# Optimization experiments

Measured on AMD Instinct MI355X. Metric: run time of the kernel, lower is better.

Reference implementation:

```python
import jax, jax.numpy as jnp
import numpy as np

N_NODES = 100000
N_EDGES = 3200000
NUM_FEATURES = 128
DIM = 10
NUM_GRAPHS = 64


def setup_inputs() -> dict:
    key = jax.random.key(0)
    k1, k2, k3, k4, k5, k6, k7 = jax.random.split(key, 7)
    features = jax.random.normal(k1, (N_NODES, NUM_FEATURES), dtype=jnp.float32)
    src = jax.random.randint(k2, (N_EDGES,), 0, N_NODES, dtype=jnp.int64)
    dst = jax.random.randint(k3, (N_EDGES,), 0, N_NODES, dtype=jnp.int64)
    graph_ids = jnp.sort(jax.random.randint(k4, (N_NODES,), 0, NUM_GRAPHS, dtype=jnp.int64))
    # GraphConv weights (no bias), glorot-ish scaling
    W1 = jax.random.normal(k5, (NUM_FEATURES, DIM), dtype=jnp.float32) / np.sqrt(NUM_FEATURES)
    W2 = jax.random.normal(k6, (DIM, DIM), dtype=jnp.float32) / np.sqrt(DIM)
    W3 = jax.random.normal(k7, (DIM, 1), dtype=jnp.float32) / np.sqrt(DIM)
    return {"features": features, "W1": W1, "W2": W2, "W3": W3,
            "src": src, "dst": dst, "graph_ids": graph_ids}


def _sum_aggregate(h, src, dst, n_nodes):
    # message = h[src], reduce-sum at dst (norm='none' GraphConv aggregation)
    return jax.ops.segment_sum(h[src], dst, num_segments=n_nodes)


def reference(features, W1, W2, W3, src, dst, graph_ids):
    n = features.shape[0]
    # conv1: in_feats(128) > out_feats(10) -> weight first, then aggregate
    h = features @ W1                          # [N, DIM]
    h = _sum_aggregate(h, src, dst, n)         # [N, DIM]
    h = jax.nn.relu(h)
    # conv2: in_feats == out_feats -> aggregate first, then weight
    h = _sum_aggregate(h, src, dst, n) @ W2    # [N, DIM]
    # dgl.mean_nodes: per-graph mean pooling over nodes
    sums = jax.ops.segment_sum(h, graph_ids, num_segments=NUM_GRAPHS)           # [G, DIM]
    cnt = jax.ops.segment_sum(jnp.ones((n, 1), h.dtype), graph_ids, num_segments=NUM_GRAPHS)
    pooled = sums / jnp.maximum(cnt, 1.0)      # [G, DIM]
    return jax.nn.sigmoid(pooled @ W3)         # [G, 1]
```

## Files before the change

kernel.cpp:

```cpp
#include <hip/hip_runtime.h>
#include <hip/hip_fp16.h>

#define N_NODES 100000
#define N_EDGES 3200000
#define NUM_FEATURES 128
#define DIM 10
#define NUM_GRAPHS 64

#define BSHIFT 8
#define BSIZE (1 << BSHIFT)
#define NB ((N_NODES + BSIZE - 1) / BSIZE)
#define CHUNKS 4
#define PCHUNKS 4
#define EPB 6250
#define PLACE_BLOCKS 512
#define NQUAD 25000
#define GEMM_BLOCKS 1563
#define BOUND_BLOCKS 196
#define TILE (BSIZE * DIM)
#define CAP 2560
#define CAPB 16384
#define NCHUNK (NB * CHUNKS)
#define NCHUNK2 (NB * PCHUNKS)
#define ACC_STRIDE 11

#define DPP_ROR_ADD(v, n)                                                        \
    (v) += __int_as_float(__builtin_amdgcn_update_dpp(                           \
        0, __float_as_int(v), 0x120 | (n), 0xF, 0xF, false))

__global__ __launch_bounds__(512) void k_front(const float* __restrict__ feat,
                                               const float* __restrict__ W1,
                                               __half* __restrict__ h1,
                                               const int* __restrict__ gids,
                                               int* __restrict__ bound,
                                               const int* __restrict__ src,
                                               const int* __restrict__ dst,
                                               int* __restrict__ cnt,
                                               int* __restrict__ pk) {
    __shared__ int hd[NB];
    __shared__ int cb[NB];

    if (blockIdx.x < PLACE_BLOCKS) {
        int base0 = blockIdx.x * EPB;
        for (int t = threadIdx.x; t < NB; t += 512) hd[t] = 0;
        __syncthreads();

        {
            int i = threadIdx.x;
            for (; i + 1536 < EPB; i += 2048) {
                int d0 = dst[base0 + i],        d1 = dst[base0 + i + 512];
                int d2 = dst[base0 + i + 1024], d3 = dst[base0 + i + 1536];
                atomicAdd(&hd[d0 >> BSHIFT], 1);
                atomicAdd(&hd[d1 >> BSHIFT], 1);
                atomicAdd(&hd[d2 >> BSHIFT], 1);
                atomicAdd(&hd[d3 >> BSHIFT], 1);
            }
            for (; i < EPB; i += 512)
                atomicAdd(&hd[dst[base0 + i] >> BSHIFT], 1);
        }
        __syncthreads();

        for (int t = threadIdx.x; t < NB; t += 512) {
            int c = hd[t];
            int o = c ? atomicAdd(&cnt[t], c) : 0;
            cb[t] = t * CAPB + o;
        }
        __syncthreads();

        {
            int i = threadIdx.x;
            for (; i + 1536 < EPB; i += 2048) {
                int d0 = dst[base0 + i],        d1 = dst[base0 + i + 512];
                int d2 = dst[base0 + i + 1024], d3 = dst[base0 + i + 1536];
                int s0 = src[base0 + i],        s1 = src[base0 + i + 512];
                int s2 = src[base0 + i + 1024], s3 = src[base0 + i + 1536];
                int q0 = atomicAdd(&cb[d0 >> BSHIFT], 1);
                int q1 = atomicAdd(&cb[d1 >> BSHIFT], 1);
                int q2 = atomicAdd(&cb[d2 >> BSHIFT], 1);
                int q3 = atomicAdd(&cb[d3 >> BSHIFT], 1);
                if (q0 < ((d0 >> BSHIFT) + 1) * CAPB) pk[q0] = ((d0 & (BSIZE - 1)) << 17) | s0;
                if (q1 < ((d1 >> BSHIFT) + 1) * CAPB) pk[q1] = ((d1 & (BSIZE - 1)) << 17) | s1;
                if (q2 < ((d2 >> BSHIFT) + 1) * CAPB) pk[q2] = ((d2 & (BSIZE - 1)) << 17) | s2;
                if (q3 < ((d3 >> BSHIFT) + 1) * CAPB) pk[q3] = ((d3 & (BSIZE - 1)) << 17) | s3;
            }
            for (; i < EPB; i += 512) {
                int d = dst[base0 + i];
                int s = src[base0 + i];
                int q = atomicAdd(&cb[d >> BSHIFT], 1);
                if (q < ((d >> BSHIFT) + 1) * CAPB) pk[q] = ((d & (BSIZE - 1)) << 17) | s;
            }
        }
        return;
    }

    int bb = blockIdx.x - PLACE_BLOCKS;

    int nb2 = bb * 512 + threadIdx.x;
    if (bb < BOUND_BLOCKS && nb2 < N_NODES) {
        int g  = gids[nb2];
        int gp = nb2 ? gids[nb2 - 1] : -1;
        for (int v = gp + 1; v <= g; ++v) bound[v] = nb2;
        if (nb2 == N_NODES - 1)
            for (int v = g + 1; v <= NUM_GRAPHS; ++v) bound[v] = N_NODES;
    }

    int gid  = bb * 512 + threadIdx.x;
    int quad = gid >> 5;
    int lane = gid & 31;
    if (quad >= NQUAD) return;

    float wf[40];
    {
        const float4* W14 = reinterpret_cast<const float4*>(W1 + lane * 40);
#pragma unroll
        for (int m = 0; m < 10; ++m) {
            float4 q = W14[m];
            wf[4 * m]     = q.x;
            wf[4 * m + 1] = q.y;
            wf[4 * m + 2] = q.z;
            wf[4 * m + 3] = q.w;
        }
    }

    int nbase = quad * 4;
    float4 f[4];
#pragma unroll
    for (int n = 0; n < 4; ++n)
        f[n] = *reinterpret_cast<const float4*>(feat + (size_t)(nbase + n) * NUM_FEATURES + lane * 4);

    float acc[4][DIM];
#pragma unroll
    for (int n = 0; n < 4; ++n)
#pragma unroll
        for (int k = 0; k < DIM; ++k) acc[n][k] = 0.f;

#pragma unroll
    for (int n = 0; n < 4; ++n) {
        float fv[4] = {f[n].x, f[n].y, f[n].z, f[n].w};
#pragma unroll
        for (int j = 0; j < 4; ++j)
#pragma unroll
            for (int k = 0; k < DIM; ++k)
                acc[n][k] += fv[j] * wf[j * DIM + k];
    }

#pragma unroll
    for (int n = 0; n < 4; ++n)
#pragma unroll
        for (int k = 0; k < DIM; ++k) {
            float v = acc[n][k];
            DPP_ROR_ADD(v, 1);
            DPP_ROR_ADD(v, 2);
            DPP_ROR_ADD(v, 4);
            DPP_ROR_ADD(v, 8);
            acc[n][k] = v + __shfl_xor(v, 16);
        }

    if (lane == 0) {
        __half2* o = (__half2*)h1;
#pragma unroll
        for (int n = 0; n < 4; ++n)
#pragma unroll
            for (int j = 0; j < 5; ++j)
                o[(size_t)(nbase + n) * 5 + j] = __floats2half2_rn(acc[n][2 * j], acc[n][2 * j + 1]);
    }
}

__global__ __launch_bounds__(512) void k_spmm1(const __half* __restrict__ h,
                                               const int* __restrict__ cnt,
                                               const int* __restrict__ pk,
                                               float* __restrict__ part) {
    __shared__ int eh[CAP];
    __shared__ int srt[CAP];
    __shared__ int hist[BSIZE];
    __shared__ int cur[BSIZE];

    int b     = blockIdx.x / CHUNKS;
    int chunk = blockIdx.x % CHUNKS;
    int s0  = b * CAPB;
    int len = cnt[b];
    int c0  = s0 + (len * chunk) / CHUNKS;
    int c1  = s0 + (len * (chunk + 1)) / CHUNKS;
    int n   = c1 - c0;
    int nc  = min(n, CAP);

    for (int t = threadIdx.x; t < BSIZE; t += 512) hist[t] = 0;
    __syncthreads();

    {
        int i = threadIdx.x;
        for (; i + 1536 < nc; i += 2048) {
            int p0 = pk[c0 + i],        p1 = pk[c0 + i + 512];
            int p2 = pk[c0 + i + 1024], p3 = pk[c0 + i + 1536];
            eh[i] = p0; eh[i + 512] = p1; eh[i + 1024] = p2; eh[i + 1536] = p3;
            atomicAdd(&hist[p0 >> 17], 1);
            atomicAdd(&hist[p1 >> 17], 1);
            atomicAdd(&hist[p2 >> 17], 1);
            atomicAdd(&hist[p3 >> 17], 1);
        }
        for (; i < nc; i += 512) {
            int p = pk[c0 + i];
            eh[i] = p;
            atomicAdd(&hist[p >> 17], 1);
        }
    }
    __syncthreads();

    if (threadIdx.x < 64) {
        int l = threadIdx.x;
        int carry = 0;
#pragma unroll
        for (int j = 0; j < 4; ++j) {
            int x = hist[j * 64 + l];
            int v = x;
#pragma unroll
            for (int off = 1; off < 64; off <<= 1) {
                int t2 = __shfl_up(v, off);
                if (l >= off) v += t2;
            }
            cur[j * 64 + l] = carry + v - x;
            carry += __shfl(v, 63);
        }
    }
    __syncthreads();

    for (int i = threadIdx.x; i < nc; i += 512) {
        int p = eh[i];
        int pos = atomicAdd(&cur[p >> 17], 1);
        srt[pos] = p;
    }
    __syncthreads();

    int wave = threadIdx.x >> 6;
    int lane = threadIdx.x & 63;
    int slot = lane / 5;
    int l    = lane - slot * 5;
    float* pb = part + (size_t)blockIdx.x * TILE;
    const __half2* h2 = (const __half2*)h;

    if (slot < 12) {
        int g = wave * 12 + slot;
        for (int loc = g; loc < BSIZE; loc += 96) {
            int e0 = loc ? cur[loc - 1] : 0;
            int e1 = cur[loc];
            float ax0 = 0.f, ay0 = 0.f, ax1 = 0.f, ay1 = 0.f;
            float ax2 = 0.f, ay2 = 0.f, ax3 = 0.f, ay3 = 0.f;
            int e = e0;
            for (; e + 7 < e1; e += 8) {
                float2 v0 = __half22float2(h2[(size_t)(srt[e]     & 0x1FFFF) * 5 + l]);
                float2 v1 = __half22float2(h2[(size_t)(srt[e + 1] & 0x1FFFF) * 5 + l]);
                float2 v2 = __half22float2(h2[(size_t)(srt[e + 2] & 0x1FFFF) * 5 + l]);
                float2 v3 = __half22float2(h2[(size_t)(srt[e + 3] & 0x1FFFF) * 5 + l]);
                float2 v4 = __half22float2(h2[(size_t)(srt[e + 4] & 0x1FFFF) * 5 + l]);
                float2 v5 = __half22float2(h2[(size_t)(srt[e + 5] & 0x1FFFF) * 5 + l]);
                float2 v6 = __half22float2(h2[(size_t)(srt[e + 6] & 0x1FFFF) * 5 + l]);
                float2 v7 = __half22float2(h2[(size_t)(srt[e + 7] & 0x1FFFF) * 5 + l]);
                ax0 += v0.x + v4.x; ay0 += v0.y + v4.y;
                ax1 += v1.x + v5.x; ay1 += v1.y + v5.y;
                ax2 += v2.x + v6.x; ay2 += v2.y + v6.y;
                ax3 += v3.x + v7.x; ay3 += v3.y + v7.y;
            }
            for (; e < e1; ++e) {
                float2 v = __half22float2(h2[(size_t)(srt[e] & 0x1FFFF) * 5 + l]);
                ax0 += v.x; ay0 += v.y;
            }
            pb[loc * DIM + 2 * l]     = (ax0 + ax1) + (ax2 + ax3);
            pb[loc * DIM + 2 * l + 1] = (ay0 + ay1) + (ay2 + ay3);
        }
    }
    __syncthreads();

    for (int i = CAP + threadIdx.x; i < n; i += 512) {
        int p = pk[c0 + i];
        int loc = p >> 17, s = p & 0x1FFFF;
#pragma unroll
        for (int j = 0; j < 5; ++j) {
            float2 v = __half22float2(h2[(size_t)s * 5 + j]);
            atomicAdd(&pb[loc * DIM + 2 * j], v.x);
            atomicAdd(&pb[loc * DIM + 2 * j + 1], v.y);
        }
    }
}

__global__ __launch_bounds__(256) void k_merge_relu(const float* __restrict__ part,
                                                    __half* __restrict__ r) {
    int b     = blockIdx.x;
    int nbase = b << BSHIFT;
    const float* p0 = part + (size_t)(b * CHUNKS) * TILE;
    __half2* r2 = (__half2*)r;
    for (int t = threadIdx.x; t < TILE / 2; t += 256) {
        float sx = 0.f, sy = 0.f;
#pragma unroll
        for (int c = 0; c < CHUNKS; ++c) {
            float2 v = ((const float2*)(p0 + (size_t)c * TILE))[t];
            sx += v.x; sy += v.y;
        }
        int ebase = nbase * DIM + 2 * t;
        if (ebase < N_NODES * DIM)
            r2[(size_t)nbase * 5 + t] = __floats2half2_rn(fmaxf(sx, 0.f), fmaxf(sy, 0.f));
    }
}

__global__ __launch_bounds__(512) void k_pass2(const __half* __restrict__ r,
                                               const int* __restrict__ cnt,
                                               const int* __restrict__ pk,
                                               const int* __restrict__ bound,
                                               float* __restrict__ sums) {
    __shared__ float acc[NUM_GRAPHS * ACC_STRIDE];

    int b     = blockIdx.x / PCHUNKS;
    int chunk = blockIdx.x % PCHUNKS;
    int nbase = b << BSHIFT;
    int nlast = min(nbase + BSIZE - 1, N_NODES - 1);

    int glo = 0, ghx = NUM_GRAPHS - 1;
#pragma unroll
    for (int it = 0; it < 6; ++it) {
        int mid = (glo + ghx + 1) >> 1;
        if (bound[mid] <= nbase) glo = mid; else ghx = mid - 1;
    }
    int lo2 = 0, hi2 = NUM_GRAPHS - 1;
#pragma unroll
    for (int it = 0; it < 6; ++it) {
        int mid = (lo2 + hi2 + 1) >> 1;
        if (bound[mid] <= nlast) lo2 = mid; else hi2 = mid - 1;
    }
    int ghi  = lo2;
    int span = ghi - glo;

    for (int t = threadIdx.x; t < (span + 1) * DIM; t += 512)
        acc[(glo + t / DIM) * ACC_STRIDE + t % DIM] = 0.f;
    __syncthreads();

    int s0  = b * CAPB;
    int len = cnt[b];
    int c0  = s0 + (len * chunk) / PCHUNKS;
    int c1  = s0 + (len * (chunk + 1)) / PCHUNKS;

    int wave = threadIdx.x >> 6;
    int lane = threadIdx.x & 63;
    int slot = lane / 5;
    int l    = lane - slot * 5;
    const __half2* r2 = (const __half2*)r;

    if (slot < 12) {
        const int STR = 96;
        int q = wave * 12 + slot;
        int e = c0 + q;
        if (span <= 1) {
            int gA  = glo;
            int gB  = (span == 1) ? glo + 1 : glo;
            int cut = (span == 1) ? (bound[glo + 1] - nbase) : BSIZE;
            float axA = 0.f, ayA = 0.f, axB = 0.f, ayB = 0.f;
            for (; e + 7 * STR < c1; e += 8 * STR) {
                int p[8];
#pragma unroll
                for (int u = 0; u < 8; ++u) p[u] = pk[e + u * STR];
                float2 v[8];
#pragma unroll
                for (int u = 0; u < 8; ++u)
                    v[u] = __half22float2(r2[(size_t)(p[u] & 0x1FFFF) * 5 + l]);
#pragma unroll
                for (int u = 0; u < 8; ++u) {
                    bool a = (p[u] >> 17) < cut;
                    axA += a ? v[u].x : 0.f;  ayA += a ? v[u].y : 0.f;
                    axB += a ? 0.f : v[u].x;  ayB += a ? 0.f : v[u].y;
                }
            }
            for (; e < c1; e += STR) {
                int p = pk[e];
                float2 v = __half22float2(r2[(size_t)(p & 0x1FFFF) * 5 + l]);
                bool a = (p >> 17) < cut;
                axA += a ? v.x : 0.f;  ayA += a ? v.y : 0.f;
                axB += a ? 0.f : v.x;  ayB += a ? 0.f : v.y;
            }
            atomicAdd(&acc[gA * ACC_STRIDE + 2 * l], axA);
            atomicAdd(&acc[gA * ACC_STRIDE + 2 * l + 1], ayA);
            if (span == 1) {
                atomicAdd(&acc[gB * ACC_STRIDE + 2 * l], axB);
                atomicAdd(&acc[gB * ACC_STRIDE + 2 * l + 1], ayB);
            }
        } else {
            for (; e < c1; e += STR) {
                int p   = pk[e];
                int loc = p >> 17;
                float2 v = __half22float2(r2[(size_t)(p & 0x1FFFF) * 5 + l]);
                int g = glo;
                for (int gg = glo + 1; gg <= ghi; ++gg)
                    g += (loc >= bound[gg] - nbase) ? 1 : 0;
                atomicAdd(&acc[g * ACC_STRIDE + 2 * l], v.x);
                atomicAdd(&acc[g * ACC_STRIDE + 2 * l + 1], v.y);
            }
        }
    }
    __syncthreads();

    for (int t = threadIdx.x; t < (span + 1) * DIM; t += 512) {
        int g = glo + t / DIM;
        float v = acc[g * ACC_STRIDE + t % DIM];
        if (v != 0.f) atomicAdd(&sums[g * DIM + t % DIM], v);
    }
}

__global__ void k_final(const float* __restrict__ sums, const int* __restrict__ bound,
                        const float* __restrict__ W2, const float* __restrict__ W3,
                        float* __restrict__ out) {
    int g = threadIdx.x;
    if (g >= NUM_GRAPHS) return;
    float c = fmaxf((float)(bound[g + 1] - bound[g]), 1.f);
    float p[DIM];
#pragma unroll
    for (int k = 0; k < DIM; ++k) p[k] = sums[g * DIM + k] / c;
    float z = 0.f;
#pragma unroll
    for (int j = 0; j < DIM; ++j) {
        float t = 0.f;
#pragma unroll
        for (int k = 0; k < DIM; ++k) t += p[k] * W2[k * DIM + j];
        z += t * W3[j];
    }
    out[g] = 1.f / (1.f + expf(-z));
}

extern "C" void kernel_launch(void* const* d_in, const int* in_sizes, int n_in,
                              void* d_out, int out_size, void* d_ws, size_t ws_size,
                              hipStream_t stream) {
    const float* feat = (const float*)d_in[0];
    const float* W1   = (const float*)d_in[1];
    const float* W2   = (const float*)d_in[2];
    const float* W3   = (const float*)d_in[3];
    const int*   src  = (const int*)d_in[4];
    const int*   dst  = (const int*)d_in[5];
    const int*   gids = (const int*)d_in[6];
    float*       out  = (float*)d_out;

    char* ws = (char*)d_ws;
    __half* h1    = (__half*)(ws);
    int*    pk    = (int*)(ws + 2000000);
    __half* r     = (__half*)(ws + 27624576);
    float*  part  = (float*)(ws + 29624576);
    int*    cnt   = (int*)(ws + 45639936);
    float*  sums  = (float*)(ws + 45641504);
    int*    bound = (int*)(ws + 45644064);

    hipMemsetAsync(ws + 45639936, 0, 4128, stream);

    k_front<<<PLACE_BLOCKS + GEMM_BLOCKS, 512, 0, stream>>>(feat, W1, h1, gids, bound,
                                                            src, dst, cnt, pk);
    k_spmm1     <<<NCHUNK, 512, 0, stream>>>(h1, cnt, pk, part);
    k_merge_relu<<<NB, 256, 0, stream>>>(part, r);
    k_pass2     <<<NCHUNK2, 512, 0, stream>>>(r, cnt, pk, bound, sums);

    k_final<<<1, 64, 0, stream>>>(sums, bound, W2, W3, out);
}
```

Measured before the change: 205.6 us.

## Bucket edges by source with graph id to compute pass2 from source-local tiles

Pass 2 only needs per-graph sums, so each edge contributes r[src] to the graph of dst. The front kernel now builds a second bucketed edge list keyed by source-node block, packing the destination's graph id. Pass 2 then loads the block's 256 rows of r into shared memory and accumulates with LDS atomics, with no random global gathers. It also changes the spmm1 chunk count and CAP. The cost is an extra histogram, an extra gids gather and a second scatter in the front kernel, plus a larger workspace.

```diff
diff --git a/kernel.cpp b/kernel.cpp
--- a/kernel.cpp
+++ b/kernel.cpp
@@ -10,18 +10,17 @@
 #define BSHIFT 8
 #define BSIZE (1 << BSHIFT)
 #define NB ((N_NODES + BSIZE - 1) / BSIZE)
-#define CHUNKS 4
-#define PCHUNKS 4
+#define CHUNKS 2
 #define EPB 6250
 #define PLACE_BLOCKS 512
 #define NQUAD 25000
 #define GEMM_BLOCKS 1563
 #define BOUND_BLOCKS 196
 #define TILE (BSIZE * DIM)
-#define CAP 2560
+#define CAP 4608
 #define CAPB 16384
+#define CAPB2 10240
 #define NCHUNK (NB * CHUNKS)
-#define NCHUNK2 (NB * PCHUNKS)
 #define ACC_STRIDE 11
 
 #define DPP_ROR_ADD(v, n)                                                        \
@@ -36,35 +35,17 @@
                                                const int* __restrict__ src,
                                                const int* __restrict__ dst,
                                                int* __restrict__ cnt,
-                                               int* __restrict__ pk) {
+                                               int* __restrict__ cnt2,
+                                               int* __restrict__ pk,
+                                               int* __restrict__ pk2) {
     __shared__ int hd[NB];
     __shared__ int cb[NB];
+    __shared__ int hs[NB];
+    __shared__ int cb2[NB];
 
     if (blockIdx.x < PLACE_BLOCKS) {
         int base0 = blockIdx.x * EPB;
-        for (int t = threadIdx.x; t < NB; t += 512) hd[t] = 0;
-        __syncthreads();
-
-        {
-            int i = threadIdx.x;
-            for (; i + 1536 < EPB; i += 2048) {
-                int d0 = dst[base0 + i],        d1 = dst[base0 + i + 512];
-                int d2 = dst[base0 + i + 1024], d3 = dst[base0 + i + 1536];
-                atomicAdd(&hd[d0 >> BSHIFT], 1);
-                atomicAdd(&hd[d1 >> BSHIFT], 1);
-                atomicAdd(&hd[d2 >> BSHIFT], 1);
-                atomicAdd(&hd[d3 >> BSHIFT], 1);
-            }
-            for (; i < EPB; i += 512)
-                atomicAdd(&hd[dst[base0 + i] >> BSHIFT], 1);
-        }
-        __syncthreads();
-
-        for (int t = threadIdx.x; t < NB; t += 512) {
-            int c = hd[t];
-            int o = c ? atomicAdd(&cnt[t], c) : 0;
-            cb[t] = t * CAPB + o;
-        }
+        for (int t = threadIdx.x; t < NB; t += 512) { hd[t] = 0; hs[t] = 0; }
         __syncthreads();
 
         {
@@ -74,6 +55,40 @@
                 int d2 = dst[base0 + i + 1024], d3 = dst[base0 + i + 1536];
                 int s0 = src[base0 + i],        s1 = src[base0 + i + 512];
                 int s2 = src[base0 + i + 1024], s3 = src[base0 + i + 1536];
+                atomicAdd(&hd[d0 >> BSHIFT], 1);
+                atomicAdd(&hd[d1 >> BSHIFT], 1);
+                atomicAdd(&hd[d2 >> BSHIFT], 1);
+                atomicAdd(&hd[d3 >> BSHIFT], 1);
+                atomicAdd(&hs[s0 >> BSHIFT], 1);
+                atomicAdd(&hs[s1 >> BSHIFT], 1);
+                atomicAdd(&hs[s2 >> BSHIFT], 1);
+                atomicAdd(&hs[s3 >> BSHIFT], 1);
+            }
+            for (; i < EPB; i += 512) {
+                atomicAdd(&hd[dst[base0 + i] >> BSHIFT], 1);
+                atomicAdd(&hs[src[base0 + i] >> BSHIFT], 1);
+            }
+        }
+        __syncthreads();
+
+        for (int t = threadIdx.x; t < NB; t += 512) {
+            int c = hd[t];
+            int o = c ? atomicAdd(&cnt[t], c) : 0;
+            cb[t] = t * CAPB + o;
+            int c2 = hs[t];
+            int o2 = c2 ? atomicAdd(&cnt2[t], c2) : 0;
+            cb2[t] = t * CAPB2 + o2;
+        }
+        __syncthreads();
+
+        {
+            int i = threadIdx.x;
+            for (; i + 1536 < EPB; i += 2048) {
+                int d0 = dst[base0 + i],        d1 = dst[base0 + i + 512];
+                int d2 = dst[base0 + i + 1024], d3 = dst[base0 + i + 1536];
+                int s0 = src[base0 + i],        s1 = src[base0 + i + 512];
+                int s2 = src[base0 + i + 1024], s3 = src[base0 + i + 1536];
+                int g0 = gids[d0], g1 = gids[d1], g2 = gids[d2], g3 = gids[d3];
                 int q0 = atomicAdd(&cb[d0 >> BSHIFT], 1);
                 int q1 = atomicAdd(&cb[d1 >> BSHIFT], 1);
                 int q2 = atomicAdd(&cb[d2 >> BSHIFT], 1);
@@ -82,12 +97,23 @@
                 if (q1 < ((d1 >> BSHIFT) + 1) * CAPB) pk[q1] = ((d1 & (BSIZE - 1)) << 17) | s1;
                 if (q2 < ((d2 >> BSHIFT) + 1) * CAPB) pk[q2] = ((d2 & (BSIZE - 1)) << 17) | s2;
                 if (q3 < ((d3 >> BSHIFT) + 1) * CAPB) pk[q3] = ((d3 & (BSIZE - 1)) << 17) | s3;
+                int w0 = atomicAdd(&cb2[s0 >> BSHIFT], 1);
+                int w1 = atomicAdd(&cb2[s1 >> BSHIFT], 1);
+                int w2 = atomicAdd(&cb2[s2 >> BSHIFT], 1);
+                int w3 = atomicAdd(&cb2[s3 >> BSHIFT], 1);
+                if (w0 < ((s0 >> BSHIFT) + 1) * CAPB2) pk2[w0] = ((s0 & (BSIZE - 1)) << 17) | g0;
+                if (w1 < ((s1 >> BSHIFT) + 1) * CAPB2) pk2[w1] = ((s1 & (BSIZE - 1)) << 17) | g1;
+                if (w2 < ((s2 >> BSHIFT) + 1) * CAPB2) pk2[w2] = ((s2 & (BSIZE - 1)) << 17) | g2;
+                if (w3 < ((s3 >> BSHIFT) + 1) * CAPB2) pk2[w3] = ((s3 & (BSIZE - 1)) << 17) | g3;
             }
             for (; i < EPB; i += 512) {
                 int d = dst[base0 + i];
                 int s = src[base0 + i];
+                int g = gids[d];
                 int q = atomicAdd(&cb[d >> BSHIFT], 1);
                 if (q < ((d >> BSHIFT) + 1) * CAPB) pk[q] = ((d & (BSIZE - 1)) << 17) | s;
+                int w = atomicAdd(&cb2[s >> BSHIFT], 1);
+                if (w < ((s >> BSHIFT) + 1) * CAPB2) pk2[w] = ((s & (BSIZE - 1)) << 17) | g;
             }
         }
         return;
@@ -302,103 +328,46 @@
 }
 
 __global__ __launch_bounds__(512) void k_pass2(const __half* __restrict__ r,
-                                               const int* __restrict__ cnt,
-                                               const int* __restrict__ pk,
-                                               const int* __restrict__ bound,
+                                               const int* __restrict__ cnt2,
+                                               const int* __restrict__ pk2,
                                                float* __restrict__ sums) {
+    __shared__ __half2 lr[BSIZE * 5];
     __shared__ float acc[NUM_GRAPHS * ACC_STRIDE];
 
-    int b     = blockIdx.x / PCHUNKS;
-    int chunk = blockIdx.x % PCHUNKS;
+    int b     = blockIdx.x;
     int nbase = b << BSHIFT;
-    int nlast = min(nbase + BSIZE - 1, N_NODES - 1);
-
-    int glo = 0, ghx = NUM_GRAPHS - 1;
-#pragma unroll
-    for (int it = 0; it < 6; ++it) {
-        int mid = (glo + ghx + 1) >> 1;
-        if (bound[mid] <= nbase) glo = mid; else ghx = mid - 1;
-    }
-    int lo2 = 0, hi2 = NUM_GRAPHS - 1;
-#pragma unroll
-    for (int it = 0; it < 6; ++it) {
-        int mid = (lo2 + hi2 + 1) >> 1;
-        if (bound[mid] <= nlast) lo2 = mid; else hi2 = mid - 1;
-    }
-    int ghi  = lo2;
-    int span = ghi - glo;
-
-    for (int t = threadIdx.x; t < (span + 1) * DIM; t += 512)
-        acc[(glo + t / DIM) * ACC_STRIDE + t % DIM] = 0.f;
-    __syncthreads();
-
-    int s0  = b * CAPB;
-    int len = cnt[b];
-    int c0  = s0 + (len * chunk) / PCHUNKS;
-    int c1  = s0 + (len * (chunk + 1)) / PCHUNKS;
-
-    int wave = threadIdx.x >> 6;
-    int lane = threadIdx.x & 63;
-    int slot = lane / 5;
-    int l    = lane - slot * 5;
+
+    for (int t = threadIdx.x; t < NUM_GRAPHS * ACC_STRIDE; t += 512) acc[t] = 0.f;
+
     const __half2* r2 = (const __half2*)r;
-
-    if (slot < 12) {
-        const int STR = 96;
-        int q = wave * 12 + slot;
-        int e = c0 + q;
-        if (span <= 1) {
-            int gA  = glo;
-            int gB  = (span == 1) ? glo + 1 : glo;
-            int cut = (span == 1) ? (bound[glo + 1] - nbase) : BSIZE;
-            float axA = 0.f, ayA = 0.f, axB = 0.f, ayB = 0.f;
-            for (; e + 7 * STR < c1; e += 8 * STR) {
-                int p[8];
-#pragma unroll
-                for (int u = 0; u < 8; ++u) p[u] = pk[e + u * STR];
-                float2 v[8];
-#pragma unroll
-                for (int u = 0; u < 8; ++u)
-                    v[u] = __half22float2(r2[(size_t)(p[u] & 0x1FFFF) * 5 + l]);
-#pragma unroll
-                for (int u = 0; u < 8; ++u) {
-                    bool a = (p[u] >> 17) < cut;
-                    axA += a ? v[u].x : 0.f;  ayA += a ? v[u].y : 0.f;
-                    axB += a ? 0.f : v[u].x;  ayB += a ? 0.f : v[u].y;
-                }
-            }
-            for (; e < c1; e += STR) {
-                int p = pk[e];
-                float2 v = __half22float2(r2[(size_t)(p & 0x1FFFF) * 5 + l]);
-                bool a = (p >> 17) < cut;
-                axA += a ? v.x : 0.f;  ayA += a ? v.y : 0.f;
-                axB += a ? 0.f : v.x;  ayB += a ? 0.f : v.y;
-            }
-            atomicAdd(&acc[gA * ACC_STRIDE + 2 * l], axA);
-            atomicAdd(&acc[gA * ACC_STRIDE + 2 * l + 1], ayA);
-            if (span == 1) {
-                atomicAdd(&acc[gB * ACC_STRIDE + 2 * l], axB);
-                atomicAdd(&acc[gB * ACC_STRIDE + 2 * l + 1], ayB);
-            }
-        } else {
-            for (; e < c1; e += STR) {
-                int p   = pk[e];
-                int loc = p >> 17;
-                float2 v = __half22float2(r2[(size_t)(p & 0x1FFFF) * 5 + l]);
-                int g = glo;
-                for (int gg = glo + 1; gg <= ghi; ++gg)
-                    g += (loc >= bound[gg] - nbase) ? 1 : 0;
-                atomicAdd(&acc[g * ACC_STRIDE + 2 * l], v.x);
-                atomicAdd(&acc[g * ACC_STRIDE + 2 * l + 1], v.y);
-            }
-        }
-    }
-    __syncthreads();
-
-    for (int t = threadIdx.x; t < (span + 1) * DIM; t += 512) {
-        int g = glo + t / DIM;
-        float v = acc[g * ACC_STRIDE + t % DIM];
-        if (v != 0.f) atomicAdd(&sums[g * DIM + t % DIM], v);
+    for (int t = threadIdx.x; t < BSIZE * 5; t += 512) {
+        int node = nbase + t / 5;
+        lr[t] = (node < N_NODES) ? r2[(size_t)node * 5 + (t - (t / 5) * 5)]
+                                 : __floats2half2_rn(0.f, 0.f);
+    }
+    __syncthreads();
+
+    int s0  = b * CAPB2;
+    int len = min(cnt2[b], CAPB2);
+    int c1  = s0 + len;
+
+    for (int e = s0 + threadIdx.x; e < c1; e += 512) {
+        int p   = pk2[e];
+        int loc = p >> 17;
+        int g   = p & 63;
+        float* ag = &acc[g * ACC_STRIDE];
+#pragma unroll
+        for (int j = 0; j < 5; ++j) {
+            float2 v = __half22float2(lr[loc * 5 + j]);
+            atomicAdd(&ag[2 * j],     v.x);
+            atomicAdd(&ag[2 * j + 1], v.y);
+        }
+    }
+    __syncthreads();
+
+    for (int t = threadIdx.x; t < NUM_GRAPHS * DIM; t += 512) {
+        float v = acc[(t / DIM) * ACC_STRIDE + (t - (t / DIM) * DIM)];
+        if (v != 0.f) atomicAdd(&sums[t], v);
     }
 }
 
@@ -437,19 +406,21 @@
     char* ws = (char*)d_ws;
     __half* h1    = (__half*)(ws);
     int*    pk    = (int*)(ws + 2000000);
-    __half* r     = (__half*)(ws + 27624576);
-    float*  part  = (float*)(ws + 29624576);
-    int*    cnt   = (int*)(ws + 45639936);
-    float*  sums  = (float*)(ws + 45641504);
-    int*    bound = (int*)(ws + 45644064);
-
-    hipMemsetAsync(ws + 45639936, 0, 4128, stream);
+    int*    pk2   = (int*)(ws + 27624576);
+    __half* r     = (__half*)(ws + 43638912);
+    float*  part  = (float*)(ws + 45638912);
+    int*    cnt   = (int*)(ws + 53646592);
+    int*    cnt2  = (int*)(ws + 53648160);
+    float*  sums  = (float*)(ws + 53649728);
+    int*    bound = (int*)(ws + 53652288);
+
+    hipMemsetAsync(ws + 53646592, 0, 5696, stream);
 
     k_front<<<PLACE_BLOCKS + GEMM_BLOCKS, 512, 0, stream>>>(feat, W1, h1, gids, bound,
-                                                            src, dst, cnt, pk);
+                                                            src, dst, cnt, cnt2, pk, pk2);
     k_spmm1     <<<NCHUNK, 512, 0, stream>>>(h1, cnt, pk, part);
     k_merge_relu<<<NB, 256, 0, stream>>>(part, r);
-    k_pass2     <<<NCHUNK2, 512, 0, stream>>>(r, cnt, pk, bound, sums);
+    k_pass2     <<<NB, 512, 0, stream>>>(r, cnt2, pk2, sums);
 
     k_final<<<1, 64, 0, stream>>>(sums, bound, W2, W3, out);
 }
```

Result: slower. 432.6 us (+110.4%).
